# Kernel optimization log

Measured on AMD Instinct MI355X. Metric: run time of the kernel, lower is better.

## Reference

```python
import jax, jax.numpy as jnp
import numpy as np

D_MODEL = 1024
NUM_HEADS = 16
HEAD_DIM = D_MODEL // NUM_HEADS


def setup_inputs() -> dict:
    key = jax.random.key(0)
    ks = jax.random.split(key, 9)
    B, S = 2, 2048
    s = 1.0 / np.sqrt(D_MODEL)
    inp = {
        "x": jax.random.normal(ks[0], (B, S, D_MODEL), dtype=jnp.float32),
        "Wq": jax.random.normal(ks[1], (D_MODEL, D_MODEL), dtype=jnp.float32) * s,
        "bq": jnp.zeros((D_MODEL,), dtype=jnp.float32),
        "Wk": jax.random.normal(ks[2], (D_MODEL, D_MODEL), dtype=jnp.float32) * s,
        "bk": jnp.zeros((D_MODEL,), dtype=jnp.float32),
        "Wv": jax.random.normal(ks[3], (D_MODEL, D_MODEL), dtype=jnp.float32) * s,
        "bv": jnp.zeros((D_MODEL,), dtype=jnp.float32),
        "Wo": jax.random.normal(ks[4], (D_MODEL, D_MODEL), dtype=jnp.float32) * s,
        "bo": jnp.zeros((D_MODEL,), dtype=jnp.float32),
    }
    return inp


def _rope(x, seq_len):
    # x: [B, H, S, Dh]; rotate-half RoPE with base 10000
    dh = x.shape[-1]
    inv_freq = 1.0 / (10000.0 ** (jnp.arange(0, dh, 2, dtype=jnp.float32) / dh))
    t = jnp.arange(seq_len, dtype=jnp.float32)
    freqs = jnp.einsum("i,j->ij", t, inv_freq)          # [S, Dh/2]
    emb = jnp.concatenate([freqs, freqs], axis=-1)        # [S, Dh]
    cos = jnp.cos(emb)[None, None, :, :]
    sin = jnp.sin(emb)[None, None, :, :]
    x1, x2 = jnp.split(x, 2, axis=-1)
    rot = jnp.concatenate([-x2, x1], axis=-1)
    return x * cos + rot * sin


def reference(x, Wq, bq, Wk, bk, Wv, bv, Wo, bo):
    B, S, _ = x.shape
    H, Dh = NUM_HEADS, HEAD_DIM

    def proj(W, b):
        y = x @ W.T + b                                   # [B, S, D]
        return y.reshape(B, S, H, Dh).transpose(0, 2, 1, 3)  # [B, H, S, Dh]

    q = _rope(proj(Wq, bq), S)
    k = _rope(proj(Wk, bk), S)
    v = proj(Wv, bv)

    scores = jnp.einsum("bhqd,bhkd->bhqk", q, k) / jnp.sqrt(jnp.float32(Dh))
    causal = jnp.triu(jnp.ones((S, S), dtype=bool), k=1)  # True above diag -> masked
    scores = jnp.where(causal[None, None], -jnp.inf, scores)
    attn = jax.nn.softmax(scores, axis=-1)
    out = jnp.einsum("bhqk,bhkd->bhqd", attn, v)          # [B, H, S, Dh]
    out = out.transpose(0, 2, 1, 3).reshape(B, S, H * Dh)
    return out @ Wo.T + bo
```

## Files before the change

kernel.cpp:

```cpp
#include <hip/hip_runtime.h>
#include <math.h>

typedef __bf16 bf16_t;
typedef bf16_t bf16x8 __attribute__((ext_vector_type(8)));
typedef float f32x4 __attribute__((ext_vector_type(4)));
typedef unsigned int u32x4 __attribute__((ext_vector_type(4)));

#define S_LEN 2048
#define NHEAD 16
#define DHEAD 64
#define DMODEL 1024
#define BATCH 2

__device__ __forceinline__ float bf2f(unsigned short u) {
    unsigned int x = ((unsigned int)u) << 16;
    return __builtin_bit_cast(float, x);
}
__device__ __forceinline__ unsigned short f2bf(float f) {
    unsigned int x = __builtin_bit_cast(unsigned int, f);
    x += 0x7fffu + ((x >> 16) & 1u);
    return (unsigned short)(x >> 16);
}

__device__ __forceinline__ void glds16(const void* g, void* l) {
    __builtin_amdgcn_global_load_lds(
        (__attribute__((address_space(1))) void*)g,
        (__attribute__((address_space(3))) void*)l,
        16, 0, 0);
}

#define SCALE2 0.1803368801f

__global__ __launch_bounds__(256) void cvt_kernel(
    const float* __restrict__ x,  const float* __restrict__ wq,
    const float* __restrict__ wk, const float* __restrict__ wv,
    const float* __restrict__ wo,
    unsigned short* __restrict__ xb,  unsigned short* __restrict__ wqb,
    unsigned short* __restrict__ wkb, unsigned short* __restrict__ wvb,
    unsigned short* __restrict__ wob)
{
    const int bid = blockIdx.x;
    const float* s;
    unsigned short* d;
    int i;
    if (bid < 4096) {
        s = x; d = xb; i = bid * 256 + threadIdx.x;
    } else {
        const int k = (bid - 4096) >> 10;
        s = (k == 0) ? wq : (k == 1) ? wk : (k == 2) ? wv : wo;
        d = (k == 0) ? wqb : (k == 1) ? wkb : (k == 2) ? wvb : wob;
        i = ((bid - 4096) & 1023) * 256 + threadIdx.x;
    }
    float4 v = ((const float4*)s)[i];
    ushort4 o;
    o.x = f2bf(v.x); o.y = f2bf(v.y); o.z = f2bf(v.z); o.w = f2bf(v.w);
    ((ushort4*)d)[i] = o;
}

__global__ __launch_bounds__(256) void rope_table_kernel(float2* __restrict__ tab)
{
    const int gid = blockIdx.x * 256 + threadIdx.x;
    const int s = gid >> 5, d = gid & 31;
    const float freq = exp2f(-0.4152410119f * (float)d);
    const float ang = (float)s * freq;
    tab[gid] = make_float2(cosf(ang), sinf(ang));
}

__global__ __launch_bounds__(256, 2) void qkv_gemm_kernel(
    const unsigned short* __restrict__ xb,
    const unsigned short* __restrict__ wqb, const unsigned short* __restrict__ wkb,
    const unsigned short* __restrict__ wvb,
    const float* __restrict__ bq, const float* __restrict__ bk, const float* __restrict__ bv,
    const float2* __restrict__ tab,
    unsigned short* __restrict__ Qr, unsigned short* __restrict__ Kr,
    unsigned short* __restrict__ VT)
{
    __shared__ __align__(16) unsigned short As[128 * 64];
    __shared__ __align__(16) unsigned short Bs[128 * 64];

    const int which = blockIdx.x >> 3;
    const int bn = (blockIdx.x & 7) * 128;
    const int bm = blockIdx.y * 128;
    const unsigned short* W = (which == 0) ? wqb : (which == 1) ? wkb : wvb;
    const float* bias       = (which == 0) ? bq  : (which == 1) ? bk  : bv;

    const int tid  = threadIdx.x;
    const int lane = tid & 63;
    const int w    = tid >> 6;
    const int quad = lane >> 4;
    const int l16  = lane & 15;
    const int wm   = (w >> 1) * 64;
    const int wn   = (w & 1) * 64;

    f32x4 acc[4][4];
#pragma unroll
    for (int i = 0; i < 4; ++i)
#pragma unroll
        for (int j = 0; j < 4; ++j)
            acc[i][j] = f32x4{0.f, 0.f, 0.f, 0.f};

    const int r8 = tid >> 3, c8 = (tid & 7) * 8;
    const unsigned short* ga = xb + (size_t)(bm + r8) * DMODEL + c8;
    const unsigned short* gb = W  + (size_t)(bn + r8) * DMODEL + c8;
    unsigned short* la = As + tid * 8;
    unsigned short* lb = Bs + tid * 8;

    for (int k0 = 0; k0 < DMODEL; k0 += 64) {
#pragma unroll
        for (int i = 0; i < 4; ++i) {
            glds16(ga + k0 + (size_t)(i * 32) * DMODEL, la + i * 2048);
            glds16(gb + k0 + (size_t)(i * 32) * DMODEL, lb + i * 2048);
        }
        __syncthreads();

        bf16x8 aF[2][4], bF[2][4];
#pragma unroll
        for (int ks = 0; ks < 2; ++ks)
#pragma unroll
            for (int t = 0; t < 4; ++t) {
                aF[ks][t] = *(const bf16x8*)(&As[(wm + t * 16 + l16) * 64 + ks * 32 + quad * 8]);
                bF[ks][t] = *(const bf16x8*)(&Bs[(wn + t * 16 + l16) * 64 + ks * 32 + quad * 8]);
            }
#pragma unroll
        for (int ks = 0; ks < 2; ++ks)
#pragma unroll
            for (int mt = 0; mt < 4; ++mt)
#pragma unroll
                for (int nt = 0; nt < 4; ++nt)
                    acc[mt][nt] = __builtin_amdgcn_mfma_f32_16x16x32_bf16(
                        aF[ks][mt], bF[ks][nt], acc[mt][nt], 0, 0, 0);
        __syncthreads();
    }

    if (which < 2) {
        unsigned short* Y = (which == 0) ? Qr : Kr;
        const float qscale = (which == 0) ? SCALE2 : 1.0f;
#pragma unroll
        for (int mt = 0; mt < 4; ++mt) {
            const int row0 = bm + wm + mt * 16 + quad * 4;
#pragma unroll
            for (int nt = 0; nt < 2; ++nt) {
                const int d   = nt * 16 + l16;
                const int col = bn + wn + nt * 16 + l16;
                const float b1 = bias[col];
                const float b2 = bias[col + 32];
#pragma unroll
                for (int r = 0; r < 4; ++r) {
                    const int row = row0 + r;
                    const int s = row & (S_LEN - 1);
                    const float2 cs = tab[s * 32 + d];
                    const float x1 = acc[mt][nt][r] + b1;
                    const float x2 = acc[mt][nt + 2][r] + b2;
                    Y[(size_t)row * DMODEL + col]      = f2bf((x1 * cs.x - x2 * cs.y) * qscale);
                    Y[(size_t)row * DMODEL + col + 32] = f2bf((x2 * cs.x + x1 * cs.y) * qscale);
                }
            }
        }
    } else {
#pragma unroll
        for (int mt = 0; mt < 4; ++mt) {
            const int row0 = bm + wm + mt * 16 + quad * 4;
            const int bb = row0 >> 11, s0 = row0 & (S_LEN - 1);
            const int h = (bn + wn) >> 6;
#pragma unroll
            for (int nt = 0; nt < 4; ++nt) {
                const int d = nt * 16 + l16;
                const float bv2 = bias[bn + wn + nt * 16 + l16];
                unsigned short pk[4];
#pragma unroll
                for (int r = 0; r < 4; ++r)
                    pk[r] = f2bf(acc[mt][nt][r] + bv2);
                *(uint2*)(&VT[((size_t)(bb * NHEAD + h) * DHEAD + d) * S_LEN + s0]) =
                    *(const uint2*)pk;
            }
        }
    }
}

__global__ __launch_bounds__(512, 4) void attn_kernel(
    const unsigned short* __restrict__ Q, const unsigned short* __restrict__ K,
    const unsigned short* __restrict__ VT, unsigned short* __restrict__ O)
{
    const int j  = blockIdx.x;
    const int bh = j & 31;
    const int qs = j >> 5;
    const int b  = bh >> 4, h = bh & 15;
    const int qt = (qs < 8) ? (15 - qs) : (qs - 8);

    const int tid  = threadIdx.x;
    const int w    = tid >> 6;
    const int lane = tid & 63;
    const int quad = lane >> 4;
    const int l16  = lane & 15;

    __shared__ __align__(16) unsigned short Ks[2][128 * 64];
    __shared__ __align__(16) unsigned short Vt[2][64 * 128];

    const int q0 = qt * 128;
    const unsigned short* Qb = Q  + (size_t)b * S_LEN * DMODEL + h * DHEAD;
    const unsigned short* Kb = K  + (size_t)b * S_LEN * DMODEL + h * DHEAD;
    const unsigned short* Vh = VT + ((size_t)(b * NHEAD + h)) * DHEAD * S_LEN;

    const int qrow = q0 + w * 16 + l16;
    const bf16x8 qf0 = *(const bf16x8*)(Qb + (size_t)qrow * DMODEL + quad * 8);
    const bf16x8 qf1 = *(const bf16x8*)(Qb + (size_t)qrow * DMODEL + 32 + quad * 8);

    f32x4 o[4];
#pragma unroll
    for (int i = 0; i < 4; ++i) o[i] = f32x4{0.f, 0.f, 0.f, 0.f};
    float l_acc = 0.f;

    const int nkt = qt + 1;

#define STAGE(bs, kt_) do {                                                        \
        _Pragma("unroll")                                                          \
        for (int i_ = 0; i_ < 2; ++i_) {                                           \
            const int ck = tid + i_ * 512;                                         \
            const int krow = ck >> 3, kc = ck & 7;                                 \
            glds16(Kb + (size_t)((kt_) * 128 + krow) * DMODEL + ((kc ^ (krow & 7)) * 8), \
                   &Ks[bs][ck * 8]);                                               \
            const int vrow = ck >> 4, vc = ck & 15;                                \
            glds16(Vh + (size_t)vrow * S_LEN + (kt_) * 128 + ((vc ^ (vrow & 15)) * 8), \
                   &Vt[bs][ck * 8]);                                               \
        }                                                                          \
    } while (0)

    STAGE(0, 0);

    for (int kt = 0; kt < nkt; ++kt) {
        const int cur = kt & 1;

        if (kt + 1 < nkt) {
            STAGE(cur ^ 1, kt + 1);
            asm volatile("s_waitcnt vmcnt(4)" ::: "memory");
        } else {
            asm volatile("s_waitcnt vmcnt(0)" ::: "memory");
        }
        __builtin_amdgcn_s_barrier();

        const bool diag = (kt == qt);
        const int ntmax = diag ? ((w & ~1) + 2) : 8;
        const int cmax  = ntmax >> 1;

        f32x4 sc[8];
#pragma unroll
        for (int nt = 0; nt < 8; ++nt) {
            if (nt >= ntmax) break;
            const int row = nt * 16 + l16;
            const bf16x8 kf0 = *(const bf16x8*)(&Ks[cur][row * 64 + ((quad ^ (l16 & 7)) * 8)]);
            const bf16x8 kf1 = *(const bf16x8*)(&Ks[cur][row * 64 + (((4 + quad) ^ (l16 & 7)) * 8)]);
            f32x4 a = f32x4{0.f, 0.f, 0.f, 0.f};
            a = __builtin_amdgcn_mfma_f32_16x16x32_bf16(kf0, qf0, a, 0, 0, 0);
            a = __builtin_amdgcn_mfma_f32_16x16x32_bf16(kf1, qf1, a, 0, 0, 0);
            sc[nt] = a;
        }

        if (diag) {
            const int thr = q0 + w * 16 + l16 - kt * 128 - quad * 4;
#pragma unroll
            for (int nt = 0; nt < 8; ++nt) {
                if (nt >= ntmax) break;
#pragma unroll
                for (int r = 0; r < 4; ++r)
                    if (nt * 16 + r > thr) sc[nt][r] = -INFINITY;
            }
        }

#pragma unroll
        for (int nt = 0; nt < 8; ++nt) {
            if (nt >= ntmax) break;
#pragma unroll
            for (int r = 0; r < 4; ++r) {
                const float e = exp2f(sc[nt][r]);
                sc[nt][r] = e;
                l_acc += e;
            }
        }

        bf16x8 pA[4];
        const bool qlo = (quad < 2);
#pragma unroll
        for (int c = 0; c < 4; ++c) {
            if (c >= cmax) break;
            unsigned int s0, s1, t0, t1;
            asm("v_cvt_pk_bf16_f32 %0, %1, %2" : "=v"(s0) : "v"(sc[2*c][0]),   "v"(sc[2*c][1]));
            asm("v_cvt_pk_bf16_f32 %0, %1, %2" : "=v"(s1) : "v"(sc[2*c][2]),   "v"(sc[2*c][3]));
            asm("v_cvt_pk_bf16_f32 %0, %1, %2" : "=v"(t0) : "v"(sc[2*c+1][0]), "v"(sc[2*c+1][1]));
            asm("v_cvt_pk_bf16_f32 %0, %1, %2" : "=v"(t1) : "v"(sc[2*c+1][2]), "v"(sc[2*c+1][3]));
            const unsigned int m0 = qlo ? s0 : t0, m1 = qlo ? s1 : t1;
            const unsigned int n0 = qlo ? t0 : s0, n1 = qlo ? t1 : s1;
            const unsigned int X0 = __shfl_xor(m0, 16), X1 = __shfl_xor(m1, 16);
            const unsigned int A0 = __shfl_xor(n0, 32), A1 = __shfl_xor(n1, 32);
            const unsigned int B0 = __shfl_xor(n0, 48), B1 = __shfl_xor(n1, 48);
            u32x4 aw;
            aw[0] = qlo ? (quad == 0 ? m0 : B0) : (quad == 2 ? A0 : X0);
            aw[1] = qlo ? (quad == 0 ? m1 : B1) : (quad == 2 ? A1 : X1);
            aw[2] = qlo ? (quad == 0 ? X0 : A0) : (quad == 2 ? B0 : m0);
            aw[3] = qlo ? (quad == 0 ? X1 : A1) : (quad == 2 ? B1 : m1);
            pA[c] = __builtin_bit_cast(bf16x8, aw);
        }

#pragma unroll
        for (int nt = 0; nt < 4; ++nt) {
            const int row = nt * 16 + l16;
#pragma unroll
            for (int c = 0; c < 4; ++c) {
                if (c >= cmax) break;
                const bf16x8 vF = *(const bf16x8*)(&Vt[cur][row * 128 + (((c * 4 + quad) ^ l16) * 8)]);
                o[nt] = __builtin_amdgcn_mfma_f32_16x16x32_bf16(pA[c], vF, o[nt], 0, 0, 0);
            }
        }

        asm volatile("s_waitcnt lgkmcnt(0)" ::: "memory");
        __builtin_amdgcn_s_barrier();
    }
#undef STAGE

    {
        float rs = l_acc;
        rs += __shfl_xor(rs, 16);
        rs += __shfl_xor(rs, 32);
        const float linv_row = 1.0f / rs;
        float linv[4];
#pragma unroll
        for (int r = 0; r < 4; ++r)
            linv[r] = __shfl(linv_row, quad * 4 + r);

        const int spos0 = q0 + w * 16 + quad * 4;
#pragma unroll
        for (int nt = 0; nt < 4; ++nt)
#pragma unroll
            for (int r = 0; r < 4; ++r) {
                const float val = o[nt][r] * linv[r];
                O[((size_t)b * S_LEN + spos0 + r) * DMODEL + h * DHEAD + nt * 16 + l16] = f2bf(val);
            }
    }
}

__global__ __launch_bounds__(256, 2) void outproj_kernel(
    const unsigned short* __restrict__ A, const unsigned short* __restrict__ W,
    const float* __restrict__ bias, float* __restrict__ C)
{
    __shared__ __align__(16) unsigned short As[64 * 64];
    __shared__ __align__(16) unsigned short Bs[128 * 64];

    const int tid  = threadIdx.x;
    const int lane = tid & 63;
    const int w    = tid >> 6;
    const int quad = lane >> 4;
    const int l16  = lane & 15;
    const int wm   = (w >> 1) * 32;
    const int wn   = (w & 1) * 64;
    const int bm   = blockIdx.y * 64;
    const int bn   = blockIdx.x * 128;

    f32x4 acc[2][4];
#pragma unroll
    for (int i = 0; i < 2; ++i)
#pragma unroll
        for (int j = 0; j < 4; ++j)
            acc[i][j] = f32x4{0.f, 0.f, 0.f, 0.f};

    const int r8 = tid >> 3, c8 = (tid & 7) * 8;
    const unsigned short* ga = A + (size_t)(bm + r8) * DMODEL + c8;
    const unsigned short* gb = W + (size_t)(bn + r8) * DMODEL + c8;
    unsigned short* la = As + tid * 8;
    unsigned short* lb = Bs + tid * 8;

    for (int k0 = 0; k0 < DMODEL; k0 += 64) {
#pragma unroll
        for (int i = 0; i < 2; ++i)
            glds16(ga + k0 + (size_t)(i * 32) * DMODEL, la + i * 2048);
#pragma unroll
        for (int i = 0; i < 4; ++i)
            glds16(gb + k0 + (size_t)(i * 32) * DMODEL, lb + i * 2048);
        __syncthreads();

        bf16x8 aF[2][2], bF[2][4];
#pragma unroll
        for (int ks = 0; ks < 2; ++ks) {
#pragma unroll
            for (int t = 0; t < 2; ++t)
                aF[ks][t] = *(const bf16x8*)(&As[(wm + t * 16 + l16) * 64 + ks * 32 + quad * 8]);
#pragma unroll
            for (int t = 0; t < 4; ++t)
                bF[ks][t] = *(const bf16x8*)(&Bs[(wn + t * 16 + l16) * 64 + ks * 32 + quad * 8]);
        }
#pragma unroll
        for (int ks = 0; ks < 2; ++ks)
#pragma unroll
            for (int mt = 0; mt < 2; ++mt)
#pragma unroll
                for (int nt = 0; nt < 4; ++nt)
                    acc[mt][nt] = __builtin_amdgcn_mfma_f32_16x16x32_bf16(
                        aF[ks][mt], bF[ks][nt], acc[mt][nt], 0, 0, 0);
        __syncthreads();
    }

#pragma unroll
    for (int mt = 0; mt < 2; ++mt) {
        const int row0 = bm + wm + mt * 16 + quad * 4;
#pragma unroll
        for (int nt = 0; nt < 4; ++nt) {
            const int col = bn + wn + nt * 16 + l16;
            const float bv = bias[col];
#pragma unroll
            for (int r = 0; r < 4; ++r)
                C[(size_t)(row0 + r) * DMODEL + col] = acc[mt][nt][r] + bv;
        }
    }
}

extern "C" void kernel_launch(void* const* d_in, const int* in_sizes, int n_in,
                              void* d_out, int out_size, void* d_ws, size_t ws_size,
                              hipStream_t stream) {
    const float* x  = (const float*)d_in[0];
    const float* Wq = (const float*)d_in[1];
    const float* bq = (const float*)d_in[2];
    const float* Wk = (const float*)d_in[3];
    const float* bk = (const float*)d_in[4];
    const float* Wv = (const float*)d_in[5];
    const float* bv = (const float*)d_in[6];
    const float* Wo = (const float*)d_in[7];
    const float* bo = (const float*)d_in[8];
    float* out = (float*)d_out;

    char* ws = (char*)d_ws;
    const size_t MB = 1 << 20;
    unsigned short* xb  = (unsigned short*)(ws);
    unsigned short* wqb = (unsigned short*)(ws + 8  * MB);
    unsigned short* wkb = (unsigned short*)(ws + 10 * MB);
    unsigned short* wvb = (unsigned short*)(ws + 12 * MB);
    unsigned short* wob = (unsigned short*)(ws + 14 * MB);
    float2*         tab = (float2*)       (ws + 16 * MB);
    unsigned short* Qr  = (unsigned short*)(ws + 17 * MB);
    unsigned short* Kr  = (unsigned short*)(ws + 25 * MB);
    unsigned short* VT  = (unsigned short*)(ws + 33 * MB);
    unsigned short* AO  = (unsigned short*)(ws + 41 * MB);

    const int M = BATCH * S_LEN;

    cvt_kernel<<<dim3(8192), 256, 0, stream>>>(
        x, Wq, Wk, Wv, Wo, xb, wqb, wkb, wvb, wob);

    rope_table_kernel<<<256, 256, 0, stream>>>(tab);

    qkv_gemm_kernel<<<dim3(24, M / 128), 256, 0, stream>>>(
        xb, wqb, wkb, wvb, bq, bk, bv, tab, Qr, Kr, VT);

    attn_kernel<<<dim3(512), 512, 0, stream>>>(Qr, Kr, VT, AO);

    outproj_kernel<<<dim3(DMODEL / 128, M / 64), 256, 0, stream>>>(AO, wob, bo, out);
}
```

Measured before the change: 196.0 us.

## Double-buffer LDS tiles in QKV and output-projection GEMMs with async prefetch

Both GEMM kernels now hold two LDS buffers per operand. Each iteration prefetches the next K-tile with direct global-to-LDS loads before computing on the current one, and uses explicit vmcnt waits so the MFMA work overlaps the memory latency. LDS use per block doubles (64KB for the QKV GEMM), which may reduce occupancy below the launch bound of two blocks. The correctness of the partial vmcnt wait depends on the instruction count per stage.

```diff
diff --git a/kernel.cpp b/kernel.cpp
--- a/kernel.cpp
+++ b/kernel.cpp
@@ -75,8 +75,8 @@
     unsigned short* __restrict__ Qr, unsigned short* __restrict__ Kr,
     unsigned short* __restrict__ VT)
 {
-    __shared__ __align__(16) unsigned short As[128 * 64];
-    __shared__ __align__(16) unsigned short Bs[128 * 64];
+    __shared__ __align__(16) unsigned short As[2][128 * 64];
+    __shared__ __align__(16) unsigned short Bs[2][128 * 64];
 
     const int which = blockIdx.x >> 3;
     const int bn = (blockIdx.x & 7) * 128;
@@ -102,24 +102,36 @@
     const int r8 = tid >> 3, c8 = (tid & 7) * 8;
     const unsigned short* ga = xb + (size_t)(bm + r8) * DMODEL + c8;
     const unsigned short* gb = W  + (size_t)(bn + r8) * DMODEL + c8;
-    unsigned short* la = As + tid * 8;
-    unsigned short* lb = Bs + tid * 8;
-
-    for (int k0 = 0; k0 < DMODEL; k0 += 64) {
-#pragma unroll
-        for (int i = 0; i < 4; ++i) {
-            glds16(ga + k0 + (size_t)(i * 32) * DMODEL, la + i * 2048);
-            glds16(gb + k0 + (size_t)(i * 32) * DMODEL, lb + i * 2048);
-        }
-        __syncthreads();
+
+#define QSTAGE(bs, k0_) do {                                                      \
+        _Pragma("unroll")                                                         \
+        for (int i_ = 0; i_ < 4; ++i_) {                                          \
+            glds16(ga + (k0_) + (size_t)(i_ * 32) * DMODEL,                       \
+                   &As[bs][tid * 8 + i_ * 2048]);                                 \
+            glds16(gb + (k0_) + (size_t)(i_ * 32) * DMODEL,                       \
+                   &Bs[bs][tid * 8 + i_ * 2048]);                                 \
+        }                                                                         \
+    } while (0)
+
+    QSTAGE(0, 0);
+
+    for (int kt = 0; kt < 16; ++kt) {
+        const int cur = kt & 1;
+        if (kt < 15) {
+            QSTAGE(cur ^ 1, (kt + 1) * 64);
+            asm volatile("s_waitcnt vmcnt(8)" ::: "memory");
+        } else {
+            asm volatile("s_waitcnt vmcnt(0)" ::: "memory");
+        }
+        __builtin_amdgcn_s_barrier();
 
         bf16x8 aF[2][4], bF[2][4];
 #pragma unroll
         for (int ks = 0; ks < 2; ++ks)
 #pragma unroll
             for (int t = 0; t < 4; ++t) {
-                aF[ks][t] = *(const bf16x8*)(&As[(wm + t * 16 + l16) * 64 + ks * 32 + quad * 8]);
-                bF[ks][t] = *(const bf16x8*)(&Bs[(wn + t * 16 + l16) * 64 + ks * 32 + quad * 8]);
+                aF[ks][t] = *(const bf16x8*)(&As[cur][(wm + t * 16 + l16) * 64 + ks * 32 + quad * 8]);
+                bF[ks][t] = *(const bf16x8*)(&Bs[cur][(wn + t * 16 + l16) * 64 + ks * 32 + quad * 8]);
             }
 #pragma unroll
         for (int ks = 0; ks < 2; ++ks)
@@ -129,8 +141,11 @@
                 for (int nt = 0; nt < 4; ++nt)
                     acc[mt][nt] = __builtin_amdgcn_mfma_f32_16x16x32_bf16(
                         aF[ks][mt], bF[ks][nt], acc[mt][nt], 0, 0, 0);
-        __syncthreads();
-    }
+
+        asm volatile("s_waitcnt lgkmcnt(0)" ::: "memory");
+        __builtin_amdgcn_s_barrier();
+    }
+#undef QSTAGE
 
     if (which < 2) {
         unsigned short* Y = (which == 0) ? Qr : Kr;
@@ -341,8 +356,8 @@
     const unsigned short* __restrict__ A, const unsigned short* __restrict__ W,
     const float* __restrict__ bias, float* __restrict__ C)
 {
-    __shared__ __align__(16) unsigned short As[64 * 64];
-    __shared__ __align__(16) unsigned short Bs[128 * 64];
+    __shared__ __align__(16) unsigned short As[2][64 * 64];
+    __shared__ __align__(16) unsigned short Bs[2][128 * 64];
 
     const int tid  = threadIdx.x;
     const int lane = tid & 63;
@@ -364,27 +379,39 @@
     const int r8 = tid >> 3, c8 = (tid & 7) * 8;
     const unsigned short* ga = A + (size_t)(bm + r8) * DMODEL + c8;
     const unsigned short* gb = W + (size_t)(bn + r8) * DMODEL + c8;
-    unsigned short* la = As + tid * 8;
-    unsigned short* lb = Bs + tid * 8;
-
-    for (int k0 = 0; k0 < DMODEL; k0 += 64) {
-#pragma unroll
-        for (int i = 0; i < 2; ++i)
-            glds16(ga + k0 + (size_t)(i * 32) * DMODEL, la + i * 2048);
-#pragma unroll
-        for (int i = 0; i < 4; ++i)
-            glds16(gb + k0 + (size_t)(i * 32) * DMODEL, lb + i * 2048);
-        __syncthreads();
+
+#define OSTAGE(bs, k0_) do {                                                      \
+        _Pragma("unroll")                                                         \
+        for (int i_ = 0; i_ < 2; ++i_)                                            \
+            glds16(ga + (k0_) + (size_t)(i_ * 32) * DMODEL,                       \
+                   &As[bs][tid * 8 + i_ * 2048]);                                 \
+        _Pragma("unroll")                                                         \
+        for (int i_ = 0; i_ < 4; ++i_)                                            \
+            glds16(gb + (k0_) + (size_t)(i_ * 32) * DMODEL,                       \
+                   &Bs[bs][tid * 8 + i_ * 2048]);                                 \
+    } while (0)
+
+    OSTAGE(0, 0);
+
+    for (int kt = 0; kt < 16; ++kt) {
+        const int cur = kt & 1;
+        if (kt < 15) {
+            OSTAGE(cur ^ 1, (kt + 1) * 64);
+            asm volatile("s_waitcnt vmcnt(6)" ::: "memory");
+        } else {
+            asm volatile("s_waitcnt vmcnt(0)" ::: "memory");
+        }
+        __builtin_amdgcn_s_barrier();
 
         bf16x8 aF[2][2], bF[2][4];
 #pragma unroll
         for (int ks = 0; ks < 2; ++ks) {
 #pragma unroll
             for (int t = 0; t < 2; ++t)
-                aF[ks][t] = *(const bf16x8*)(&As[(wm + t * 16 + l16) * 64 + ks * 32 + quad * 8]);
+                aF[ks][t] = *(const bf16x8*)(&As[cur][(wm + t * 16 + l16) * 64 + ks * 32 + quad * 8]);
 #pragma unroll
             for (int t = 0; t < 4; ++t)
-                bF[ks][t] = *(const bf16x8*)(&Bs[(wn + t * 16 + l16) * 64 + ks * 32 + quad * 8]);
+                bF[ks][t] = *(const bf16x8*)(&Bs[cur][(wn + t * 16 + l16) * 64 + ks * 32 + quad * 8]);
         }
 #pragma unroll
         for (int ks = 0; ks < 2; ++ks)
@@ -394,8 +421,11 @@
                 for (int nt = 0; nt < 4; ++nt)
                     acc[mt][nt] = __builtin_amdgcn_mfma_f32_16x16x32_bf16(
                         aF[ks][mt], bF[ks][nt], acc[mt][nt], 0, 0, 0);
-        __syncthreads();
-    }
+
+        asm volatile("s_waitcnt lgkmcnt(0)" ::: "memory");
+        __builtin_amdgcn_s_barrier();
+    }
+#undef OSTAGE
 
 #pragma unroll
     for (int mt = 0; mt < 2; ++mt) {
```

Measured after the change: 212.1 us. +8.2%, slower.
